# Kernel tuning notes

Measured on AMD Instinct MI355X. Metric: run time of the kernel, lower is better.

Reference implementation:

```python
import jax, jax.numpy as jnp
import numpy as np

N_NODES = 100000
N_EDGES = 3200000
N_SG = 800000  # edges in the softmax-normalized segment
RULES = 9

SUB_MAT = np.array([[-0.2, -0.1, -0.05, -0.05, -0.05, -0.01, -0.055, -0.01, 0.0],
                    [0.0, -0.002, -0.001, -0.001, -0.001, -0.0002, 0.0008, -0.0002, 0.0]], dtype=np.float32)
SUB_BIAS = np.array([1, 0.7, 0.275, 0.4, 0.25, 0.07, 0.2225, 0.07, 0], dtype=np.float32)


def setup_inputs() -> dict:
    key = jax.random.key(0)
    k1, k2, k3 = jax.random.split(key, 3)
    feat = jax.random.normal(k1, (N_NODES, 4), dtype=jnp.float32)
    src = jax.random.randint(k2, (N_EDGES,), 0, N_NODES)
    dst = jax.random.randint(k3, (N_EDGES,), 0, N_NODES)
    edge_sg_ID = jnp.arange(N_SG, dtype=jnp.int64 if jax.config.read('jax_enable_x64') else jnp.int32).reshape(1, N_SG)
    return {
        'feat': feat,
        'src': src,
        'dst': dst,
        'edge_sg_ID': edge_sg_ID,
        'sub_systems_mat': jnp.asarray(SUB_MAT),
        'sub_systems_bias': jnp.asarray(SUB_BIAS),
    }


def _gauss(x, mean, sigma):
    return jnp.exp(-(x - mean) ** 2 / (2.0 * sigma ** 2))


def _ante_generator(vector):
    # vector: [E, 4] = (dpos_x, dpos_y, dvel_x, dvel_y)
    d = vector[:, :2]
    v = vector[:, 2:]
    x1 = jnp.linalg.norm(d, axis=1, keepdims=True)  # distance, [E,1]
    vnorm = jnp.linalg.norm(v, axis=1, keepdims=True)
    cos = jnp.sum(d * v, axis=1, keepdims=True) / (x1 * vnorm + 1e-8)
    x2 = jnp.degrees(jnp.arccos(jnp.clip(cos, -1.0 + 1e-6, 1.0 - 1e-6)))  # angle deg, [E,1]
    return x1, x2


def _ante_process(x1, x2):
    # memberships: x1 small/med/large, x2 small/med/large
    m1 = [_gauss(x1, 0.0, 0.75), _gauss(x1, 2.0, 0.75), _gauss(x1, 4.0, 0.75)]
    m2 = [_gauss(x2, 0.0, 30.0), _gauss(x2, 90.0, 30.0), _gauss(x2, 180.0, 30.0)]
    # 9 rules: min over all (x1_level, x2_level) pairs -> [E, 1, 9]
    return jnp.stack([jnp.minimum(a, b) for a in m1 for b in m2], axis=2)


def _forward(feat, sub_systems_mat, sub_systems_bias, src, dst, edge_sg_ID):
    vector = feat[dst] - feat[src]  # [E, 4]
    x1, x2 = _ante_generator(vector)  # each [E, 1]
    truth = _ante_process(x1, x2)  # [E, 1, 9]
    premises = jnp.stack((x1, x2), axis=2).reshape(-1, 2)  # [E, 2]
    consequence = premises @ sub_systems_mat + sub_systems_bias  # [E, 9]
    consequence = consequence.reshape(x1.shape[0], x1.shape[1], RULES)  # [E, 1, 9]
    attention = jnp.sum(truth * consequence, axis=2) / jnp.sum(truth, axis=2)  # [E, 1]
    attention = attention[:, :, None]  # [E, 1, 1]
    idx = edge_sg_ID[0]
    # segment softmax over the selected edges (dim 0)
    attention = attention.at[idx].set(jax.nn.softmax(attention[idx], axis=0))
    return attention


def reference(feat, src, dst, edge_sg_ID, sub_systems_mat, sub_systems_bias):
    return _forward(feat, sub_systems_mat, sub_systems_bias, src, dst, edge_sg_ID)
```

## Files before the change

kernel.cpp:

```cpp
#include <hip/hip_runtime.h>
#include <hip/hip_cooperative_groups.h>

namespace cg = cooperative_groups;

#define N_EDGES 3200000
#define N_SG    800000
#define RULES   9
#define BLOCK   256
#define GRID    1024
#define NT      (GRID * BLOCK)
#define TOT_GROUPS (N_EDGES / 4)
#define SG_GROUPS  (N_SG / 4)
#define FULL3      (3 * NT)
#define TAILN      (TOT_GROUPS - FULL3)
#define TAIL_PER_BLK 14

typedef float vf4 __attribute__((ext_vector_type(4)));
typedef int   vi4 __attribute__((ext_vector_type(4)));


__device__ __forceinline__ float fast_acos_deg(float x)
{
    float ax = fabsf(x);
    float p = fmaf(ax, -0.0187293f, 0.0742610f);
    p = fmaf(p, ax, -0.2121144f);
    p = fmaf(p, ax, 1.5707288f);
    float r = __builtin_amdgcn_sqrtf(1.0f - ax) * p;
    r = (x < 0.0f) ? (3.14159265358979f - r) : r;
    return r * 57.29577951308232f;
}

__device__ __forceinline__ float edge_attn(vf4 fd, vf4 fs,
                                           const float* c1, const float* c2,
                                           const float* cb)
{
    float d0 = fd.x - fs.x, d1 = fd.y - fs.y;
    float v0 = fd.z - fs.z, v1 = fd.w - fs.w;

    float d2  = fmaf(d0, d0, d1 * d1);
    float v2  = fmaf(v0, v0, v1 * v1);
    float x1  = __builtin_amdgcn_sqrtf(d2);
    float dot = fmaf(d0, v0, d1 * v1);
    float cosv = dot * __builtin_amdgcn_rcpf(
                     __builtin_amdgcn_sqrtf(d2 * v2) + 1e-8f);
    cosv = fminf(fmaxf(cosv, -1.0f + 1e-6f), 1.0f - 1e-6f);
    float x2 = fast_acos_deg(cosv);

    const float k1 = 0.888888888888889f;
    const float k2 = 5.555555555555556e-4f;
    float m1[3], m2[3];
    float a;
    a = x1;          m1[0] = __expf(-a * a * k1);
    a = x1 - 2.0f;   m1[1] = __expf(-a * a * k1);
    a = x1 - 4.0f;   m1[2] = __expf(-a * a * k1);
    a = x2;          m2[0] = __expf(-a * a * k2);
    a = x2 - 90.0f;  m2[1] = __expf(-a * a * k2);
    a = x2 - 180.0f; m2[2] = __expf(-a * a * k2);

    float num = 0.0f, den = 0.0f;
#pragma unroll
    for (int i = 0; i < 3; ++i) {
#pragma unroll
        for (int j = 0; j < 3; ++j) {
            int r = i * 3 + j;
            float t = fminf(m1[i], m2[j]);
            float c = fmaf(x1, c1[r], fmaf(x2, c2[r], cb[r]));
            num = fmaf(t, c, num);
            den += t;
        }
    }
    return num * __builtin_amdgcn_rcpf(den);
}

__device__ __forceinline__ vf4 attn_group(vi4 s, vi4 d, const vf4* feat,
                                          const float* c1, const float* c2,
                                          const float* cb)
{
    vf4 a0 = feat[s.x], a1 = feat[s.y], a2 = feat[s.z], a3 = feat[s.w];
    vf4 b0 = feat[d.x], b1 = feat[d.y], b2 = feat[d.z], b3 = feat[d.w];
    vf4 r;
    r.x = edge_attn(b0, a0, c1, c2, cb);
    r.y = edge_attn(b1, a1, c1, c2, cb);
    r.z = edge_attn(b2, a2, c1, c2, cb);
    r.w = edge_attn(b3, a3, c1, c2, cb);
    return r;
}

__global__ __launch_bounds__(BLOCK, 4) void fused_kernel(
    const vf4*   __restrict__ feat,
    const vi4*   __restrict__ src4,
    const vi4*   __restrict__ dst4,
    const float* __restrict__ M,
    const float* __restrict__ B,
    vf4*         __restrict__ out4,
    float*       __restrict__ partials)
{
    cg::grid_group grid = cg::this_grid();
    const int t = blockIdx.x * BLOCK + threadIdx.x;

    float c1[RULES], c2[RULES], cb[RULES];
#pragma unroll
    for (int r = 0; r < RULES; ++r) {
        c1[r] = M[r];
        c2[r] = M[RULES + r];
        cb[r] = B[r];
    }

    const int g0 = t, g1 = t + NT, g2 = t + 2 * NT;
    vi4 s0 = __builtin_nontemporal_load(&src4[g0]);
    vi4 d0 = __builtin_nontemporal_load(&dst4[g0]);
    vi4 s1 = __builtin_nontemporal_load(&src4[g1]);
    vi4 d1 = __builtin_nontemporal_load(&dst4[g1]);
    vi4 s2 = __builtin_nontemporal_load(&src4[g2]);
    vi4 d2 = __builtin_nontemporal_load(&dst4[g2]);

    vf4 a0 = feat[s0.x], a1 = feat[s0.y], a2 = feat[s0.z], a3 = feat[s0.w];
    vf4 b0 = feat[d0.x], b1 = feat[d0.y], b2 = feat[d0.z], b3 = feat[d0.w];
    vf4 e0 = feat[s1.x], e1 = feat[s1.y], e2 = feat[s1.z], e3 = feat[s1.w];
    vf4 f0 = feat[d1.x], f1 = feat[d1.y], f2 = feat[d1.z], f3 = feat[d1.w];

    vf4 ra;
    ra.x = edge_attn(b0, a0, c1, c2, cb);
    ra.y = edge_attn(b1, a1, c1, c2, cb);
    ra.z = edge_attn(b2, a2, c1, c2, cb);
    ra.w = edge_attn(b3, a3, c1, c2, cb);

    float s = 0.0f;
    const bool soft = (t < SG_GROUPS);
    if (soft) {
        ra.x = __expf(ra.x); ra.y = __expf(ra.y);
        ra.z = __expf(ra.z); ra.w = __expf(ra.w);
        s = (ra.x + ra.y) + (ra.z + ra.w);
    } else {
        __builtin_nontemporal_store(ra, &out4[g0]);
    }

    vf4 rb;
    rb.x = edge_attn(f0, e0, c1, c2, cb);
    rb.y = edge_attn(f1, e1, c1, c2, cb);
    rb.z = edge_attn(f2, e2, c1, c2, cb);
    rb.w = edge_attn(f3, e3, c1, c2, cb);
    __builtin_nontemporal_store(rb, &out4[g1]);

    vf4 rc = attn_group(s2, d2, feat, c1, c2, cb);
    __builtin_nontemporal_store(rc, &out4[g2]);

    if (threadIdx.x < TAIL_PER_BLK) {
        int e = blockIdx.x * TAIL_PER_BLK + threadIdx.x;
        if (e < TAILN) {
            int g = FULL3 + e;
            vi4 sr = __builtin_nontemporal_load(&src4[g]);
            vi4 dr = __builtin_nontemporal_load(&dst4[g]);
            vf4 rr = attn_group(sr, dr, feat, c1, c2, cb);
            __builtin_nontemporal_store(rr, &out4[g]);
        }
    }

    __shared__ float wsum[BLOCK / 64];
    __shared__ float stot;
#pragma unroll
    for (int o = 32; o > 0; o >>= 1) s += __shfl_down(s, o, 64);
    if ((threadIdx.x & 63) == 0) wsum[threadIdx.x >> 6] = s;
    __syncthreads();
    if (threadIdx.x == 0)
        partials[blockIdx.x] = wsum[0] + wsum[1] + wsum[2] + wsum[3];

    grid.sync();

    float ts = partials[threadIdx.x]
             + partials[threadIdx.x + 256]
             + partials[threadIdx.x + 512]
             + partials[threadIdx.x + 768];
#pragma unroll
    for (int o = 32; o > 0; o >>= 1) ts += __shfl_down(ts, o, 64);
    if ((threadIdx.x & 63) == 0) wsum[threadIdx.x >> 6] = ts;
    __syncthreads();
    if (threadIdx.x == 0) stot = wsum[0] + wsum[1] + wsum[2] + wsum[3];
    __syncthreads();

    if (soft) {
        float inv = 1.0f / stot;
        ra.x *= inv; ra.y *= inv; ra.z *= inv; ra.w *= inv;
        out4[g0] = ra;
    }
}

#define FB_THREADS (N_EDGES / 8)
#define FB_BLOCKS  ((FB_THREADS + BLOCK - 1) / BLOCK)
#define FB_SOFT    (N_SG / 8)
#define FB_K2_BLKS ((SG_GROUPS + BLOCK - 1) / BLOCK)

__global__ __launch_bounds__(BLOCK, 4) void fb_edge_kernel(
    const vf4* __restrict__ feat, const vi4* __restrict__ src4,
    const vi4* __restrict__ dst4, const float* __restrict__ M,
    const float* __restrict__ B, vf4* __restrict__ out4,
    float* __restrict__ partials)
{
    int t = blockIdx.x * BLOCK + threadIdx.x;
    float s = 0.0f;
    float c1[RULES], c2[RULES], cb[RULES];
#pragma unroll
    for (int r = 0; r < RULES; ++r) {
        c1[r] = M[r]; c2[r] = M[RULES + r]; cb[r] = B[r];
    }
    if (t < FB_THREADS) {
        vi4 sa = src4[2 * t], sb = src4[2 * t + 1];
        vi4 da = dst4[2 * t], db = dst4[2 * t + 1];
        vf4 ra = attn_group(sa, da, feat, c1, c2, cb);
        vf4 rb = attn_group(sb, db, feat, c1, c2, cb);
        if (t < FB_SOFT) {
            ra.x = __expf(ra.x); ra.y = __expf(ra.y);
            ra.z = __expf(ra.z); ra.w = __expf(ra.w);
            rb.x = __expf(rb.x); rb.y = __expf(rb.y);
            rb.z = __expf(rb.z); rb.w = __expf(rb.w);
            s = (ra.x + ra.y + ra.z + ra.w) + (rb.x + rb.y + rb.z + rb.w);
        }
        out4[2 * t] = ra;
        out4[2 * t + 1] = rb;
    }
#pragma unroll
    for (int o = 32; o > 0; o >>= 1) s += __shfl_down(s, o, 64);
    __shared__ float wsum[BLOCK / 64];
    if ((threadIdx.x & 63) == 0) wsum[threadIdx.x >> 6] = s;
    __syncthreads();
    if (threadIdx.x == 0)
        partials[blockIdx.x] = wsum[0] + wsum[1] + wsum[2] + wsum[3];
}

__global__ __launch_bounds__(BLOCK) void fb_softmax_kernel(
    const float* __restrict__ partials, vf4* __restrict__ out4)
{
    float s = 0.0f;
    for (int p = threadIdx.x; p < FB_BLOCKS; p += BLOCK) s += partials[p];
#pragma unroll
    for (int o = 32; o > 0; o >>= 1) s += __shfl_down(s, o, 64);
    __shared__ float wsum[BLOCK / 64];
    if ((threadIdx.x & 63) == 0) wsum[threadIdx.x >> 6] = s;
    __syncthreads();
    float inv = 1.0f / (wsum[0] + wsum[1] + wsum[2] + wsum[3]);
    int i = blockIdx.x * BLOCK + threadIdx.x;
    if (i < SG_GROUPS) {
        vf4 v = out4[i];
        v.x *= inv; v.y *= inv; v.z *= inv; v.w *= inv;
        out4[i] = v;
    }
}

extern "C" void kernel_launch(void* const* d_in, const int* in_sizes, int n_in,
                              void* d_out, int out_size, void* d_ws, size_t ws_size,
                              hipStream_t stream)
{
    const vf4*   feat = (const vf4*)d_in[0];
    const vi4*   src4 = (const vi4*)d_in[1];
    const vi4*   dst4 = (const vi4*)d_in[2];
    const float* M    = (const float*)d_in[4];
    const float* B    = (const float*)d_in[5];
    vf4*   out4     = (vf4*)d_out;
    float* partials = (float*)d_ws;

    int bpc = 0;
    hipOccupancyMaxActiveBlocksPerMultiprocessor(&bpc,
        (const void*)fused_kernel, BLOCK, 0);

    if (bpc >= 4) {
        void* args[] = {
            (void*)&feat, (void*)&src4, (void*)&dst4,
            (void*)&M, (void*)&B, (void*)&out4, (void*)&partials
        };
        hipLaunchCooperativeKernel((const void*)fused_kernel,
                                   dim3(GRID), dim3(BLOCK), args, 0, stream);
    } else {
        fb_edge_kernel<<<dim3(FB_BLOCKS), dim3(BLOCK), 0, stream>>>(
            feat, src4, dst4, M, B, out4, partials);
        fb_softmax_kernel<<<dim3(FB_K2_BLKS), dim3(BLOCK), 0, stream>>>(
            partials, out4);
    }
}
```

Baseline: 119.2 us.

## Replace cooperative grid-sync kernel with two plain launches and one-group-per-thread

Drops the cooperative launch with a grid-wide barrier and the per-call occupancy query. In their place come an edge kernel that handles one 4-edge group per thread over a full-size grid, and a separate scale kernel that normalizes the softmax segment. The aim is to remove grid.sync latency and host-side occupancy-query overhead, and to let the hardware schedule more blocks at higher occupancy. The cost is a second kernel launch and a re-read and re-write of the 800K softmax outputs, where before they were scaled in registers.

```diff
diff --git a/kernel.cpp b/kernel.cpp
--- a/kernel.cpp
+++ b/kernel.cpp
@@ -1,23 +1,18 @@
 #include <hip/hip_runtime.h>
-#include <hip/hip_cooperative_groups.h>
 
-namespace cg = cooperative_groups;
 
 #define N_EDGES 3200000
 #define N_SG    800000
 #define RULES   9
 #define BLOCK   256
-#define GRID    1024
-#define NT      (GRID * BLOCK)
 #define TOT_GROUPS (N_EDGES / 4)
 #define SG_GROUPS  (N_SG / 4)
-#define FULL3      (3 * NT)
-#define TAILN      (TOT_GROUPS - FULL3)
-#define TAIL_PER_BLK 14
+#define GRID1      (TOT_GROUPS / BLOCK)
+#define NSOFTBLK   ((SG_GROUPS + BLOCK - 1) / BLOCK)
+#define GRID2      NSOFTBLK
 
 typedef float vf4 __attribute__((ext_vector_type(4)));
 typedef int   vi4 __attribute__((ext_vector_type(4)));
-
 
 __device__ __forceinline__ float fast_acos_deg(float x)
 {
@@ -72,21 +67,7 @@
     return num * __builtin_amdgcn_rcpf(den);
 }
 
-__device__ __forceinline__ vf4 attn_group(vi4 s, vi4 d, const vf4* feat,
-                                          const float* c1, const float* c2,
-                                          const float* cb)
-{
-    vf4 a0 = feat[s.x], a1 = feat[s.y], a2 = feat[s.z], a3 = feat[s.w];
-    vf4 b0 = feat[d.x], b1 = feat[d.y], b2 = feat[d.z], b3 = feat[d.w];
-    vf4 r;
-    r.x = edge_attn(b0, a0, c1, c2, cb);
-    r.y = edge_attn(b1, a1, c1, c2, cb);
-    r.z = edge_attn(b2, a2, c1, c2, cb);
-    r.w = edge_attn(b3, a3, c1, c2, cb);
-    return r;
-}
-
-__global__ __launch_bounds__(BLOCK, 4) void fused_kernel(
+__global__ __launch_bounds__(BLOCK, 8) void edge_kernel(
     const vf4*   __restrict__ feat,
     const vi4*   __restrict__ src4,
     const vi4*   __restrict__ dst4,
@@ -95,8 +76,10 @@
     vf4*         __restrict__ out4,
     float*       __restrict__ partials)
 {
-    cg::grid_group grid = cg::this_grid();
     const int t = blockIdx.x * BLOCK + threadIdx.x;
+
+    vi4 s0 = __builtin_nontemporal_load(&src4[t]);
+    vi4 d0 = __builtin_nontemporal_load(&dst4[t]);
 
     float c1[RULES], c2[RULES], cb[RULES];
 #pragma unroll
@@ -106,143 +89,59 @@
         cb[r] = B[r];
     }
 
-    const int g0 = t, g1 = t + NT, g2 = t + 2 * NT;
-    vi4 s0 = __builtin_nontemporal_load(&src4[g0]);
-    vi4 d0 = __builtin_nontemporal_load(&dst4[g0]);
-    vi4 s1 = __builtin_nontemporal_load(&src4[g1]);
-    vi4 d1 = __builtin_nontemporal_load(&dst4[g1]);
-    vi4 s2 = __builtin_nontemporal_load(&src4[g2]);
-    vi4 d2 = __builtin_nontemporal_load(&dst4[g2]);
-
     vf4 a0 = feat[s0.x], a1 = feat[s0.y], a2 = feat[s0.z], a3 = feat[s0.w];
     vf4 b0 = feat[d0.x], b1 = feat[d0.y], b2 = feat[d0.z], b3 = feat[d0.w];
-    vf4 e0 = feat[s1.x], e1 = feat[s1.y], e2 = feat[s1.z], e3 = feat[s1.w];
-    vf4 f0 = feat[d1.x], f1 = feat[d1.y], f2 = feat[d1.z], f3 = feat[d1.w];
 
-    vf4 ra;
-    ra.x = edge_attn(b0, a0, c1, c2, cb);
-    ra.y = edge_attn(b1, a1, c1, c2, cb);
-    ra.z = edge_attn(b2, a2, c1, c2, cb);
-    ra.w = edge_attn(b3, a3, c1, c2, cb);
+    vf4 r;
+    r.x = edge_attn(b0, a0, c1, c2, cb);
+    r.y = edge_attn(b1, a1, c1, c2, cb);
+    r.z = edge_attn(b2, a2, c1, c2, cb);
+    r.w = edge_attn(b3, a3, c1, c2, cb);
 
     float s = 0.0f;
     const bool soft = (t < SG_GROUPS);
     if (soft) {
-        ra.x = __expf(ra.x); ra.y = __expf(ra.y);
-        ra.z = __expf(ra.z); ra.w = __expf(ra.w);
-        s = (ra.x + ra.y) + (ra.z + ra.w);
+        r.x = __expf(r.x); r.y = __expf(r.y);
+        r.z = __expf(r.z); r.w = __expf(r.w);
+        s = (r.x + r.y) + (r.z + r.w);
+        out4[t] = r;
     } else {
-        __builtin_nontemporal_store(ra, &out4[g0]);
+        __builtin_nontemporal_store(r, &out4[t]);
     }
 
-    vf4 rb;
-    rb.x = edge_attn(f0, e0, c1, c2, cb);
-    rb.y = edge_attn(f1, e1, c1, c2, cb);
-    rb.z = edge_attn(f2, e2, c1, c2, cb);
-    rb.w = edge_attn(f3, e3, c1, c2, cb);
-    __builtin_nontemporal_store(rb, &out4[g1]);
+    if (blockIdx.x < NSOFTBLK) {
+#pragma unroll
+        for (int o = 32; o > 0; o >>= 1) s += __shfl_down(s, o, 64);
+        __shared__ float wsum[BLOCK / 64];
+        if ((threadIdx.x & 63) == 0) wsum[threadIdx.x >> 6] = s;
+        __syncthreads();
+        if (threadIdx.x == 0)
+            partials[blockIdx.x] = wsum[0] + wsum[1] + wsum[2] + wsum[3];
+    }
+}
 
-    vf4 rc = attn_group(s2, d2, feat, c1, c2, cb);
-    __builtin_nontemporal_store(rc, &out4[g2]);
-
-    if (threadIdx.x < TAIL_PER_BLK) {
-        int e = blockIdx.x * TAIL_PER_BLK + threadIdx.x;
-        if (e < TAILN) {
-            int g = FULL3 + e;
-            vi4 sr = __builtin_nontemporal_load(&src4[g]);
-            vi4 dr = __builtin_nontemporal_load(&dst4[g]);
-            vf4 rr = attn_group(sr, dr, feat, c1, c2, cb);
-            __builtin_nontemporal_store(rr, &out4[g]);
-        }
-    }
+__global__ __launch_bounds__(BLOCK, 8) void scale_kernel(
+    const float* __restrict__ partials,
+    vf4*         __restrict__ out4)
+{
+    float s = 0.0f;
+    for (int p = threadIdx.x; p < NSOFTBLK; p += BLOCK) s += partials[p];
+#pragma unroll
+    for (int o = 32; o > 0; o >>= 1) s += __shfl_down(s, o, 64);
 
     __shared__ float wsum[BLOCK / 64];
     __shared__ float stot;
-#pragma unroll
-    for (int o = 32; o > 0; o >>= 1) s += __shfl_down(s, o, 64);
     if ((threadIdx.x & 63) == 0) wsum[threadIdx.x >> 6] = s;
-    __syncthreads();
-    if (threadIdx.x == 0)
-        partials[blockIdx.x] = wsum[0] + wsum[1] + wsum[2] + wsum[3];
-
-    grid.sync();
-
-    float ts = partials[threadIdx.x]
-             + partials[threadIdx.x + 256]
-             + partials[threadIdx.x + 512]
-             + partials[threadIdx.x + 768];
-#pragma unroll
-    for (int o = 32; o > 0; o >>= 1) ts += __shfl_down(ts, o, 64);
-    if ((threadIdx.x & 63) == 0) wsum[threadIdx.x >> 6] = ts;
     __syncthreads();
     if (threadIdx.x == 0) stot = wsum[0] + wsum[1] + wsum[2] + wsum[3];
     __syncthreads();
 
-    if (soft) {
-        float inv = 1.0f / stot;
-        ra.x *= inv; ra.y *= inv; ra.z *= inv; ra.w *= inv;
-        out4[g0] = ra;
-    }
-}
-
-#define FB_THREADS (N_EDGES / 8)
-#define FB_BLOCKS  ((FB_THREADS + BLOCK - 1) / BLOCK)
-#define FB_SOFT    (N_SG / 8)
-#define FB_K2_BLKS ((SG_GROUPS + BLOCK - 1) / BLOCK)
-
-__global__ __launch_bounds__(BLOCK, 4) void fb_edge_kernel(
-    const vf4* __restrict__ feat, const vi4* __restrict__ src4,
-    const vi4* __restrict__ dst4, const float* __restrict__ M,
-    const float* __restrict__ B, vf4* __restrict__ out4,
-    float* __restrict__ partials)
-{
-    int t = blockIdx.x * BLOCK + threadIdx.x;
-    float s = 0.0f;
-    float c1[RULES], c2[RULES], cb[RULES];
-#pragma unroll
-    for (int r = 0; r < RULES; ++r) {
-        c1[r] = M[r]; c2[r] = M[RULES + r]; cb[r] = B[r];
-    }
-    if (t < FB_THREADS) {
-        vi4 sa = src4[2 * t], sb = src4[2 * t + 1];
-        vi4 da = dst4[2 * t], db = dst4[2 * t + 1];
-        vf4 ra = attn_group(sa, da, feat, c1, c2, cb);
-        vf4 rb = attn_group(sb, db, feat, c1, c2, cb);
-        if (t < FB_SOFT) {
-            ra.x = __expf(ra.x); ra.y = __expf(ra.y);
-            ra.z = __expf(ra.z); ra.w = __expf(ra.w);
-            rb.x = __expf(rb.x); rb.y = __expf(rb.y);
-            rb.z = __expf(rb.z); rb.w = __expf(rb.w);
-            s = (ra.x + ra.y + ra.z + ra.w) + (rb.x + rb.y + rb.z + rb.w);
-        }
-        out4[2 * t] = ra;
-        out4[2 * t + 1] = rb;
-    }
-#pragma unroll
-    for (int o = 32; o > 0; o >>= 1) s += __shfl_down(s, o, 64);
-    __shared__ float wsum[BLOCK / 64];
-    if ((threadIdx.x & 63) == 0) wsum[threadIdx.x >> 6] = s;
-    __syncthreads();
-    if (threadIdx.x == 0)
-        partials[blockIdx.x] = wsum[0] + wsum[1] + wsum[2] + wsum[3];
-}
-
-__global__ __launch_bounds__(BLOCK) void fb_softmax_kernel(
-    const float* __restrict__ partials, vf4* __restrict__ out4)
-{
-    float s = 0.0f;
-    for (int p = threadIdx.x; p < FB_BLOCKS; p += BLOCK) s += partials[p];
-#pragma unroll
-    for (int o = 32; o > 0; o >>= 1) s += __shfl_down(s, o, 64);
-    __shared__ float wsum[BLOCK / 64];
-    if ((threadIdx.x & 63) == 0) wsum[threadIdx.x >> 6] = s;
-    __syncthreads();
-    float inv = 1.0f / (wsum[0] + wsum[1] + wsum[2] + wsum[3]);
-    int i = blockIdx.x * BLOCK + threadIdx.x;
+    const float inv = 1.0f / stot;
+    const int i = blockIdx.x * BLOCK + threadIdx.x;
     if (i < SG_GROUPS) {
         vf4 v = out4[i];
         v.x *= inv; v.y *= inv; v.z *= inv; v.w *= inv;
-        out4[i] = v;
+        __builtin_nontemporal_store(v, &out4[i]);
     }
 }
 
@@ -258,21 +157,7 @@
     vf4*   out4     = (vf4*)d_out;
     float* partials = (float*)d_ws;
 
-    int bpc = 0;
-    hipOccupancyMaxActiveBlocksPerMultiprocessor(&bpc,
-        (const void*)fused_kernel, BLOCK, 0);
-
-    if (bpc >= 4) {
-        void* args[] = {
-            (void*)&feat, (void*)&src4, (void*)&dst4,
-            (void*)&M, (void*)&B, (void*)&out4, (void*)&partials
-        };
-        hipLaunchCooperativeKernel((const void*)fused_kernel,
-                                   dim3(GRID), dim3(BLOCK), args, 0, stream);
-    } else {
-        fb_edge_kernel<<<dim3(FB_BLOCKS), dim3(BLOCK), 0, stream>>>(
-            feat, src4, dst4, M, B, out4, partials);
-        fb_softmax_kernel<<<dim3(FB_K2_BLKS), dim3(BLOCK), 0, stream>>>(
-            partials, out4);
-    }
+    edge_kernel<<<dim3(GRID1), dim3(BLOCK), 0, stream>>>(
+        feat, src4, dst4, M, B, out4, partials);
+    scale_kernel<<<dim3(GRID2), dim3(BLOCK), 0, stream>>>(partials, out4);
 }
```

Result: no change. 119.8 us (+0.5%).
